# Optimization experiments

Measured on AMD Instinct MI355X. Metric: run time of the kernel, lower is better.

Reference implementation:

```python
import jax, jax.numpy as jnp
import numpy as np

NUM_SITES = 64
BOND_DIM = 64
PHYS_DIM = 2
BATCH = 8192
INIT_STD = 0.125  # 1/sqrt(bond_dim)
EPS_AMP = 1e-12
EPS_LOG = 1e-30


def setup_inputs() -> dict:
    key = jax.random.key(0)
    k_cfg, k_l, k_b, k_r = jax.random.split(key, 4)
    configurations = jax.random.randint(k_cfg, (BATCH, NUM_SITES), 0, PHYS_DIM, dtype=jnp.int32)
    left = jax.random.normal(k_l, (PHYS_DIM, BOND_DIM), dtype=jnp.float32) * INIT_STD
    bulk = jax.random.normal(k_b, (NUM_SITES - 2, BOND_DIM, PHYS_DIM, BOND_DIM), dtype=jnp.float32) * INIT_STD
    right = jax.random.normal(k_r, (BOND_DIM, PHYS_DIM), dtype=jnp.float32) * INIT_STD
    return {"configurations": configurations, "left": left, "bulk": bulk, "right": right}


def _psi(configurations, left, bulk, right):
    # configurations: [B, S] int; left: [d, D]; bulk: [S-2, D, d, D]; right: [D, d]
    B = configurations.shape[0]
    env0 = left[configurations[:, 0]]  # [B, D]
    cfg_mid = configurations[:, 1:-1].T  # [S-2, B]

    def step(env, xs):
        site_t, idx = xs  # site_t: [D, d, D], idx: [B]
        D = site_t.shape[0]
        # env @ site (contract left bond), then gather the per-sample physical slice
        tmp = (env @ site_t.reshape(D, -1)).reshape(B, PHYS_DIM, D)  # [B, d, D]
        env = jnp.take_along_axis(tmp, idx[:, None, None], axis=1)[:, 0, :]  # [B, D]
        return env, None

    env, _ = jax.lax.scan(step, env0, (bulk, cfg_mid))
    cols = jnp.take(right, configurations[:, -1], axis=1).T  # [B, D]
    return jnp.sum(env * cols, axis=1)  # [B]


def _log_norm(left, bulk, right):
    env0 = left.T @ left  # [D, D]  (real dtype -> conj trivial)

    def step(carry, site_t):
        env, log_scale = carry
        sm = jnp.transpose(site_t, (1, 0, 2))  # [d, D, D]
        env = jnp.einsum('pdi,de,pej->ij', sm, env, sm)  # sum_p A_p^H env A_p
        scale = jnp.maximum(jnp.max(jnp.abs(env)), EPS_LOG)
        return (env / scale, log_scale + jnp.log(scale)), None

    (env, log_scale), _ = jax.lax.scan(step, (env0, jnp.zeros((), left.dtype)), bulk)
    z = jnp.sum(right * (env @ right))
    return jnp.log(jnp.maximum(z, EPS_LOG)) + log_scale


def reference(configurations, left, bulk, right):
    psi = _psi(configurations, left, bulk, right)
    abs_sq = jnp.maximum(psi * psi, EPS_AMP)
    log_z = _log_norm(left, bulk, right)
    nll = -(jnp.log(abs_sq) - log_z)
    return jnp.mean(nll)
```

## Files before the change

kernel.cpp:

```cpp
#include <hip/hip_runtime.h>
#include <math.h>

#define NBULK 62
#define SB    72
#define NPSI  128
#define NBLK  130

typedef __attribute__((ext_vector_type(8))) short bf8_t;
typedef __attribute__((ext_vector_type(4))) float f4_t;

#define MFMA(a, b, c) __builtin_amdgcn_mfma_f32_16x16x32_bf16((a), (b), (c), 0, 0, 0)

__device__ __forceinline__ unsigned short f2bf(float f) {
    unsigned int u = __float_as_uint(f);
    return (unsigned short)((u + 0x7FFFu + ((u >> 16) & 1u)) >> 16);
}
__device__ __forceinline__ float bf2f(unsigned short h) {
    return __uint_as_float(((unsigned int)h) << 16);
}

#define WS_E_OFF   1024
#define WS_B_OFF   6144
#define WS_BT_OFF  45056
#define WS_MR_OFF  1060864


extern "C" __global__ __launch_bounds__(256)
void mps_precompute(const float* __restrict__ bulkG,
                    unsigned short* __restrict__ BTg,
                    unsigned short* __restrict__ MRg,
                    float* __restrict__ wsF)
{
    __shared__ unsigned short BTl[8192];
    __shared__ unsigned short MRl[8192];
    const int s = blockIdx.x, tid = threadIdx.x;
    if (s == 0 && tid == 0) {
        wsF[0] = 0.f; wsF[1] = 0.f; wsF[2] = 0.f;
        ((int*)wsF)[3] = 0;
    }
    const float4* src = (const float4*)(bulkG + (size_t)s * 8192);
    for (int c = 0; c < 8; ++c) {
        int idx = tid + c * 256;
        float4 v = src[idx];
        int f  = idx * 4;
        int kk = f >> 7;
        int p  = (f >> 6) & 1;
        int j  = f & 63;
        unsigned short b0 = f2bf(v.x), b1 = f2bf(v.y), b2 = f2bf(v.z), b3 = f2bf(v.w);
        int n = p * 64 + kk;
        int off = n * 64 + (((j >> 3) ^ (n & 7)) << 3) + (j & 7);
        MRl[off + 0] = b0; MRl[off + 1] = b1; MRl[off + 2] = b2; MRl[off + 3] = b3;
        unsigned short bb[4] = {b0, b1, b2, b3};
        #pragma unroll
        for (int t2 = 0; t2 < 4; ++t2) {
            int n2 = p * 64 + j + t2;
            BTl[n2 * 64 + (((kk >> 3) ^ (n2 & 7)) << 3) + (kk & 7)] = bb[t2];
        }
    }
    __syncthreads();
    const uint4* bt4 = (const uint4*)BTl;
    const uint4* mr4 = (const uint4*)MRl;
    uint4* btg = (uint4*)(BTg + (size_t)s * 8192);
    uint4* mrg = (uint4*)(MRg + (size_t)s * 8192);
    for (int c = 0; c < 4; ++c) {
        int idx = tid + c * 256;
        btg[idx] = bt4[idx];
        mrg[idx] = mr4[idx];
    }
}

extern "C" __global__ __launch_bounds__(256, 1)
void mps_main(const int* __restrict__ cfgG, const float* __restrict__ leftG,
              const float* __restrict__ rightG, float* __restrict__ wsF,
              const unsigned short* __restrict__ BTg,
              const unsigned short* __restrict__ MRg,
              float* __restrict__ outG)
{
    extern __shared__ char smem[];
    unsigned short* smem16 = (unsigned short*)smem;
    const int tid  = threadIdx.x;
    const int bid  = blockIdx.x;
    const int wv   = tid >> 6;
    const int lane = tid & 63;
    const int quad = lane >> 4;
    const int ln   = lane & 15;

    if (bid >= 2) {
        unsigned short* env  = smem16;
        unsigned char*  selT = (unsigned char*)(env + 64 * SB);

        const int s0 = (bid - 2) * 64;
        {
            int m = tid >> 2, part = tid & 3;
            const int* row = cfgG + (size_t)(s0 + m) * 64 + part * 16;
            #pragma unroll
            for (int q = 0; q < 4; ++q) {
                int4 v = *(const int4*)(row + q * 4);
                int cb = part * 16 + q * 4;
                selT[(cb + 0) * 64 + m] = (unsigned char)v.x;
                selT[(cb + 1) * 64 + m] = (unsigned char)v.y;
                selT[(cb + 2) * 64 + m] = (unsigned char)v.z;
                selT[(cb + 3) * 64 + m] = (unsigned char)v.w;
            }
        }
        __syncthreads();

        int boff[2][4][2];
        #pragma unroll
        for (int b2 = 0; b2 < 2; ++b2)
            #pragma unroll
            for (int ct = 0; ct < 4; ++ct) {
                int row = b2 * 64 + ct * 16 + ln;
                #pragma unroll
                for (int h = 0; h < 2; ++h)
                    boff[b2][ct][h] = row * 64 + (((h * 4 + quad) ^ (ln & 7)) << 3);
            }

        bf8_t Af0, Af1;
        {
            int sel0 = selT[0 * 64 + wv * 16 + ln];
            const float* lp0 = leftG + sel0 * 64;
            bf8_t t0, t1;
            #pragma unroll
            for (int j = 0; j < 8; ++j) {
                t0[j] = (short)f2bf(lp0[quad * 8 + j]);
                t1[j] = (short)f2bf(lp0[32 + quad * 8 + j]);
            }
            Af0 = t0; Af1 = t1;
        }

        auto loadB = [&](bf8_t (&B)[2][4][2], int t) {
            const unsigned short* base = BTg + (size_t)t * 8192;
            #pragma unroll
            for (int b2 = 0; b2 < 2; ++b2)
                #pragma unroll
                for (int ct = 0; ct < 4; ++ct)
                    #pragma unroll
                    for (int h = 0; h < 2; ++h)
                        B[b2][ct][h] = *(const bf8_t*)(base + boff[b2][ct][h]);
        };
        auto psite = [&](bf8_t (&B)[2][4][2], int t) {
            f4_t acc[2][4];
            #pragma unroll
            for (int b2 = 0; b2 < 2; ++b2)
                #pragma unroll
                for (int ct = 0; ct < 4; ++ct) {
                    f4_t a = {0.f, 0.f, 0.f, 0.f};
                    a = MFMA(Af0, B[b2][ct][0], a);
                    a = MFMA(Af1, B[b2][ct][1], a);
                    acc[b2][ct] = a;
                }
            unsigned int sv = *(const unsigned int*)(selT + (t + 1) * 64 + wv * 16 + quad * 4);
            #pragma unroll
            for (int ct = 0; ct < 4; ++ct)
                #pragma unroll
                for (int r = 0; r < 4; ++r) {
                    float v = ((sv >> (8 * r)) & 1u) ? acc[1][ct][r] : acc[0][ct][r];
                    env[(wv * 16 + quad * 4 + r) * SB + ct * 16 + ln] = f2bf(v);
                }
            Af0 = *(const bf8_t*)(env + (wv * 16 + ln) * SB + quad * 8);
            Af1 = *(const bf8_t*)(env + (wv * 16 + ln) * SB + 32 + quad * 8);
        };

        bf8_t BfA[2][4][2], BfB[2][4][2];
        loadB(BfA, 0);
        for (int tt = 0; tt < 31; ++tt) {
            loadB(BfB, 2 * tt + 1);
            psite(BfA, 2 * tt);
            if (tt < 30) loadB(BfA, 2 * tt + 2);
            psite(BfB, 2 * tt + 1);
        }
        {
            int selL = selT[63 * 64 + wv * 16 + ln];
            bf8_t e0 = *(const bf8_t*)(env + (wv * 16 + ln) * SB + quad * 16);
            bf8_t e1 = *(const bf8_t*)(env + (wv * 16 + ln) * SB + quad * 16 + 8);
            float p = 0.f;
            #pragma unroll
            for (int j = 0; j < 8; ++j)
                p = fmaf(bf2f((unsigned short)e0[j]), rightG[(quad * 16 + j) * 2 + selL], p);
            #pragma unroll
            for (int j = 0; j < 8; ++j)
                p = fmaf(bf2f((unsigned short)e1[j]), rightG[(quad * 16 + 8 + j) * 2 + selL], p);
            p += __shfl_xor(p, 16);
            p += __shfl_xor(p, 32);
            float lp = logf(fmaxf(p * p, 1e-12f));
            lp += __shfl_xor(lp, 1); lp += __shfl_xor(lp, 2);
            lp += __shfl_xor(lp, 4); lp += __shfl_xor(lp, 8);
            if (lane == 0) atomicAdd(&wsF[0], lp);
        }
    } else {
        unsigned short* Ebf = smem16;
        unsigned short* St0 = Ebf + 64 * SB;
        unsigned short* St1 = St0 + 64 * SB;
        float* wred = (float*)(St1 + 64 * SB);

        const bool fwd = (bid == 0);
        const unsigned short* srcbase = fwd ? BTg : MRg;
        {
            int i = tid >> 2, jq = tid & 3;
            for (int jj = 0; jj < 16; ++jj) {
                int j = jq * 16 + jj;
                float v;
                if (fwd) v = leftG[i] * leftG[j] + leftG[64 + i] * leftG[64 + j];
                else     v = rightG[i * 2] * rightG[j * 2] + rightG[i * 2 + 1] * rightG[j * 2 + 1];
                Ebf[i * SB + j] = f2bf(v);
            }
        }
        float lsum = 0.f;
        const int p   = wv >> 1;
        const int ntb = (wv & 1) * 2;
        const int mta = (wv >> 1) * 2;
        const int nta = (wv & 1) * 2;
        unsigned short* Stp = p ? St1 : St0;

        int o1[2][2], o2[2][2][2];
        #pragma unroll
        for (int c = 0; c < 2; ++c) {
            int row = p * 64 + (ntb + c) * 16 + ln;
            #pragma unroll
            for (int h = 0; h < 2; ++h)
                o1[c][h] = row * 64 + (((h * 4 + quad) ^ (ln & 7)) << 3);
        }
        #pragma unroll
        for (int pp = 0; pp < 2; ++pp)
            #pragma unroll
            for (int mi = 0; mi < 2; ++mi) {
                int row = pp * 64 + (mta + mi) * 16 + ln;
                #pragma unroll
                for (int h = 0; h < 2; ++h)
                    o2[pp][mi][h] = row * 64 + (((h * 4 + quad) ^ (ln & 7)) << 3);
            }

        auto loadM = [&](bf8_t (&M1)[2][2], bf8_t (&M2)[2][2][2], int site) {
            const unsigned short* base = srcbase + (size_t)site * 8192;
            #pragma unroll
            for (int c = 0; c < 2; ++c)
                #pragma unroll
                for (int h = 0; h < 2; ++h)
                    M1[c][h] = *(const bf8_t*)(base + o1[c][h]);
            #pragma unroll
            for (int pp = 0; pp < 2; ++pp)
                #pragma unroll
                for (int mi = 0; mi < 2; ++mi)
                    #pragma unroll
                    for (int h = 0; h < 2; ++h)
                        M2[pp][mi][h] = *(const bf8_t*)(base + o2[pp][mi][h]);
        };
        auto nsite = [&](bf8_t (&M1)[2][2], bf8_t (&M2)[2][2][2],
                         bf8_t (&N1)[2][2], bf8_t (&N2)[2][2][2], int k, bool pf) {
            __syncthreads();
            float inv = 1.f;
            if (k > 0) {
                const float* wp = wred + ((k - 1) & 1) * 4;
                float mm = fmaxf(fmaxf(wp[0], wp[1]), fmaxf(wp[2], wp[3]));
                float sc = fmaxf(mm, 1e-30f);
                inv = 1.f / sc;
                if (tid == 0) lsum += logf(sc);
            }
            if (pf) loadM(N1, N2, fwd ? (k + 1) : (61 - (k + 1)));
            {
                bf8_t Af2[4][2];
                #pragma unroll
                for (int mt = 0; mt < 4; ++mt)
                    #pragma unroll
                    for (int h = 0; h < 2; ++h)
                        Af2[mt][h] = *(const bf8_t*)(Ebf + (mt * 16 + ln) * SB + h * 32 + quad * 8);
                #pragma unroll
                for (int c = 0; c < 2; ++c) {
                    int nt = ntb + c;
                    #pragma unroll
                    for (int mt = 0; mt < 4; ++mt) {
                        f4_t a = {0.f, 0.f, 0.f, 0.f};
                        a = MFMA(Af2[mt][0], M1[c][0], a);
                        a = MFMA(Af2[mt][1], M1[c][1], a);
                        ushort4 pk;
                        pk.x = f2bf(a[0]); pk.y = f2bf(a[1]); pk.z = f2bf(a[2]); pk.w = f2bf(a[3]);
                        *(ushort4*)(Stp + (nt * 16 + ln) * SB + mt * 16 + quad * 4) = pk;
                    }
                }
            }
            __syncthreads();
            {
                bf8_t Bw[2][2][2];
                #pragma unroll
                for (int pp = 0; pp < 2; ++pp)
                    #pragma unroll
                    for (int ni = 0; ni < 2; ++ni)
                        #pragma unroll
                        for (int h = 0; h < 2; ++h)
                            Bw[pp][ni][h] = *(const bf8_t*)((pp ? St1 : St0)
                                            + ((nta + ni) * 16 + ln) * SB + h * 32 + quad * 8);
                float mx = 0.f;
                #pragma unroll
                for (int mi = 0; mi < 2; ++mi)
                    #pragma unroll
                    for (int ni = 0; ni < 2; ++ni) {
                        f4_t a = {0.f, 0.f, 0.f, 0.f};
                        #pragma unroll
                        for (int pp = 0; pp < 2; ++pp)
                            #pragma unroll
                            for (int h = 0; h < 2; ++h)
                                a = MFMA(M2[pp][mi][h], Bw[pp][ni][h], a);
                        #pragma unroll
                        for (int r = 0; r < 4; ++r) {
                            float val = a[r] * inv;
                            mx = fmaxf(mx, fabsf(val));
                            Ebf[((mta + mi) * 16 + quad * 4 + r) * SB + (nta + ni) * 16 + ln] = f2bf(val);
                        }
                    }
                #pragma unroll
                for (int off = 32; off > 0; off >>= 1)
                    mx = fmaxf(mx, __shfl_xor(mx, off));
                if (lane == 0) wred[(k & 1) * 4 + wv] = mx;
            }
        };

        bf8_t M1A[2][2], M2A[2][2][2], M1B[2][2], M2B[2][2][2];
        loadM(M1A, M2A, fwd ? 0 : 61);
        for (int kk = 0; kk < 15; ++kk) {
            nsite(M1A, M2A, M1B, M2B, 2 * kk,     true);
            nsite(M1B, M2B, M1A, M2A, 2 * kk + 1, true);
        }
        nsite(M1A, M2A, M1B, M2B, 30, false);

        __syncthreads();
        float* dst = wsF + (fwd ? WS_E_OFF : WS_B_OFF);
        for (int c = 0; c < 16; ++c) {
            int idx = tid + c * 256;
            dst[idx] = bf2f(Ebf[(idx >> 6) * SB + (idx & 63)]);
        }
        if (tid == 0) wsF[fwd ? 1 : 2] = lsum;
    }

    __syncthreads();
    __threadfence();
    __syncthreads();
    int* eflag = (int*)smem;
    if (tid == 0) {
        int old = atomicAdd((int*)wsF + 3, 1);
        eflag[0] = (old == NBLK - 1) ? 1 : 0;
    }
    __syncthreads();
    if (eflag[0]) {
        __threadfence();
        const float4* E  = (const float4*)(wsF + WS_E_OFF);
        const float4* Bm = (const float4*)(wsF + WS_B_OFF);
        float a = 0.f;
        #pragma unroll
        for (int c = 0; c < 4; ++c) {
            int idx = tid + c * 256;
            float4 e = E[idx], b = Bm[idx];
            a += e.x * b.x + e.y * b.y + e.z * b.z + e.w * b.w;
        }
        #pragma unroll
        for (int off = 32; off > 0; off >>= 1)
            a += __shfl_down(a, off);
        float* ered = (float*)smem + 8;
        if ((tid & 63) == 0) ered[tid >> 6] = a;
        __syncthreads();
        if (tid == 0) {
            float z = fmaxf(ered[0] + ered[1] + ered[2] + ered[3], 1e-30f);
            float log_z = logf(z) + wsF[1] + wsF[2];
            outG[0] = log_z - wsF[0] * (1.0f / 8192.0f);
        }
    }
}

extern "C" void kernel_launch(void* const* d_in, const int* in_sizes, int n_in,
                              void* d_out, int out_size, void* d_ws, size_t ws_size,
                              hipStream_t stream)
{
    const int*   cfg   = (const int*)d_in[0];
    const float* left  = (const float*)d_in[1];
    const float* bulk  = (const float*)d_in[2];
    const float* right = (const float*)d_in[3];
    float* wsF = (float*)d_ws;
    unsigned short* BTg = (unsigned short*)((char*)d_ws + WS_BT_OFF);
    unsigned short* MRg = (unsigned short*)((char*)d_ws + WS_MR_OFF);

    mps_precompute<<<dim3(62), dim3(256), 0, stream>>>(bulk, BTg, MRg, wsF);
    mps_main<<<dim3(NBLK), dim3(256), 28672, stream>>>(cfg, left, right, wsF, BTg, MRg, (float*)d_out);
}
```

Before: 123.0 us.

## Pre-multiply adjacent MPS site pairs to halve sequential contraction steps

A precompute kernel now multiplies pairs of adjacent bulk tensors into four 64x64 product matrices per pair (one per physical index combination), so the psi chain and the norm chain each take 31 or fewer sequential steps instead of 62. The psi blocks stage each pair tile through LDS with register prefetch and select among four products using a combined 2-bit selector. The norm blocks contract over four physical combinations per step. This removes half of the latency-bound serial steps at the cost of twice the MFMA work per step, an extra bf16 rounding of the pair products (a precision change), and a larger LDS footprint.

```diff
diff --git a/kernel.cpp b/kernel.cpp
--- a/kernel.cpp
+++ b/kernel.cpp
@@ -1,15 +1,14 @@
 #include <hip/hip_runtime.h>
 #include <math.h>
 
-#define NBULK 62
-#define SB    72
-#define NPSI  128
+#define NPAIR 31
 #define NBLK  130
 
 typedef __attribute__((ext_vector_type(8))) short bf8_t;
 typedef __attribute__((ext_vector_type(4))) float f4_t;
 
 #define MFMA(a, b, c) __builtin_amdgcn_mfma_f32_16x16x32_bf16((a), (b), (c), 0, 0, 0)
+#define LGKM_BARRIER() asm volatile("s_waitcnt lgkmcnt(0)\n\ts_barrier" ::: "memory")
 
 __device__ __forceinline__ unsigned short f2bf(float f) {
     unsigned int u = __float_as_uint(f);
@@ -19,61 +18,90 @@
     return __uint_as_float(((unsigned int)h) << 16);
 }
 
-#define WS_E_OFF   1024
-#define WS_B_OFF   6144
-#define WS_BT_OFF  45056
-#define WS_MR_OFF  1060864
-
+#define WS_E_OFF 1024
+#define WS_B_OFF 6144
+#define WS_PBT   45056
+#define WS_PMR   1060864
 
 extern "C" __global__ __launch_bounds__(256)
-void mps_precompute(const float* __restrict__ bulkG,
-                    unsigned short* __restrict__ BTg,
-                    unsigned short* __restrict__ MRg,
-                    float* __restrict__ wsF)
+void mps_pre(const float* __restrict__ bulkG, unsigned short* __restrict__ PBTg,
+             unsigned short* __restrict__ PMRg, float* __restrict__ wsF)
 {
-    __shared__ unsigned short BTl[8192];
-    __shared__ unsigned short MRl[8192];
-    const int s = blockIdx.x, tid = threadIdx.x;
-    if (s == 0 && tid == 0) {
-        wsF[0] = 0.f; wsF[1] = 0.f; wsF[2] = 0.f;
-        ((int*)wsF)[3] = 0;
+    extern __shared__ char smem[];
+    unsigned short* S = (unsigned short*)smem;
+    const int t = blockIdx.x, tid = threadIdx.x;
+    const int wv = tid >> 6, lane = tid & 63, quad = lane >> 4, ln = lane & 15;
+    if (t == 0 && tid == 0) { wsF[0] = 0.f; wsF[1] = 0.f; wsF[2] = 0.f; ((int*)wsF)[3] = 0; }
+
+    unsigned short* Arow = S;
+    unsigned short* Bbt  = S + 8192;
+    const float4* sA = (const float4*)(bulkG + (size_t)(2 * t) * 8192);
+    const float4* sB = (const float4*)(bulkG + (size_t)(2 * t + 1) * 8192);
+    for (int it = 0; it < 8; ++it) {
+        int idx = tid + it * 256;
+        int f = idx * 4, kk = f >> 7, p = (f >> 6) & 1, j = f & 63;
+        float4 va = sA[idx];
+        ushort4 pa; pa.x = f2bf(va.x); pa.y = f2bf(va.y); pa.z = f2bf(va.z); pa.w = f2bf(va.w);
+        *(ushort4*)(Arow + p * 4096 + kk * 64 + (((j >> 3) ^ (kk & 7)) << 3) + (j & 7)) = pa;
+        float4 vb = sB[idx];
+        unsigned short bb[4] = {f2bf(vb.x), f2bf(vb.y), f2bf(vb.z), f2bf(vb.w)};
+        #pragma unroll
+        for (int r2 = 0; r2 < 4; ++r2) {
+            int n = j + r2;
+            Bbt[p * 4096 + n * 64 + (((kk >> 3) ^ (n & 7)) << 3) + (kk & 7)] = bb[r2];
+        }
     }
-    const float4* src = (const float4*)(bulkG + (size_t)s * 8192);
-    for (int c = 0; c < 8; ++c) {
-        int idx = tid + c * 256;
-        float4 v = src[idx];
-        int f  = idx * 4;
-        int kk = f >> 7;
-        int p  = (f >> 6) & 1;
-        int j  = f & 63;
-        unsigned short b0 = f2bf(v.x), b1 = f2bf(v.y), b2 = f2bf(v.z), b3 = f2bf(v.w);
-        int n = p * 64 + kk;
-        int off = n * 64 + (((j >> 3) ^ (n & 7)) << 3) + (j & 7);
-        MRl[off + 0] = b0; MRl[off + 1] = b1; MRl[off + 2] = b2; MRl[off + 3] = b3;
-        unsigned short bb[4] = {b0, b1, b2, b3};
-        #pragma unroll
-        for (int t2 = 0; t2 < 4; ++t2) {
-            int n2 = p * 64 + j + t2;
-            BTl[n2 * 64 + (((kk >> 3) ^ (n2 & 7)) << 3) + (kk & 7)] = bb[t2];
-        }
-    }
-    __syncthreads();
-    const uint4* bt4 = (const uint4*)BTl;
-    const uint4* mr4 = (const uint4*)MRl;
-    uint4* btg = (uint4*)(BTg + (size_t)s * 8192);
-    uint4* mrg = (uint4*)(MRg + (size_t)s * 8192);
-    for (int c = 0; c < 4; ++c) {
-        int idx = tid + c * 256;
-        btg[idx] = bt4[idx];
-        mrg[idx] = mr4[idx];
+    __syncthreads();
+    const int a = wv & 1, b = wv >> 1;
+    bf8_t Af[4][2], Bf[4][2];
+    #pragma unroll
+    for (int mt = 0; mt < 4; ++mt)
+        #pragma unroll
+        for (int h = 0; h < 2; ++h) {
+            Af[mt][h] = *(const bf8_t*)(Arow + a * 4096 + (mt * 16 + ln) * 64 + (((h * 4 + quad) ^ (ln & 7)) << 3));
+            Bf[mt][h] = *(const bf8_t*)(Bbt  + b * 4096 + (mt * 16 + ln) * 64 + (((h * 4 + quad) ^ (ln & 7)) << 3));
+        }
+    __syncthreads();
+    f4_t acc[4][4];
+    #pragma unroll
+    for (int mt = 0; mt < 4; ++mt)
+        #pragma unroll
+        for (int nt = 0; nt < 4; ++nt) {
+            f4_t x = {0.f, 0.f, 0.f, 0.f};
+            x = MFMA(Af[mt][0], Bf[nt][0], x);
+            x = MFMA(Af[mt][1], Bf[nt][1], x);
+            acc[mt][nt] = x;
+        }
+    unsigned short* Pr = S;
+    unsigned short* Pt = S + 16384;
+    #pragma unroll
+    for (int mt = 0; mt < 4; ++mt)
+        #pragma unroll
+        for (int nt = 0; nt < 4; ++nt)
+            #pragma unroll
+            for (int r = 0; r < 4; ++r) {
+                int row = mt * 16 + quad * 4 + r, col = nt * 16 + ln;
+                unsigned short v = f2bf(acc[mt][nt][r]);
+                Pr[wv * 4096 + row * 64 + (((col >> 3) ^ (row & 7)) << 3) + (col & 7)] = v;
+                Pt[wv * 4096 + col * 64 + (((row >> 3) ^ (col & 7)) << 3) + (row & 7)] = v;
+            }
+    __syncthreads();
+    const uint4* pr4 = (const uint4*)Pr;
+    const uint4* pt4 = (const uint4*)Pt;
+    uint4* mr = (uint4*)(PMRg + (size_t)t * 16384);
+    uint4* bt = (uint4*)(PBTg + (size_t)t * 16384);
+    for (int it = 0; it < 8; ++it) {
+        int idx = tid + it * 256;
+        mr[idx] = pr4[idx];
+        bt[idx] = pt4[idx];
     }
 }
 
 extern "C" __global__ __launch_bounds__(256, 1)
 void mps_main(const int* __restrict__ cfgG, const float* __restrict__ leftG,
               const float* __restrict__ rightG, float* __restrict__ wsF,
-              const unsigned short* __restrict__ BTg,
-              const unsigned short* __restrict__ MRg,
+              const unsigned short* __restrict__ PBTg,
+              const unsigned short* __restrict__ PMRg,
               float* __restrict__ outG)
 {
     extern __shared__ char smem[];
@@ -86,8 +114,10 @@
     const int ln   = lane & 15;
 
     if (bid >= 2) {
-        unsigned short* env  = smem16;
-        unsigned char*  selT = (unsigned char*)(env + 64 * SB);
+        unsigned short* tile = smem16;
+        unsigned short* env  = tile + 16384;
+        unsigned char*  selT = (unsigned char*)(env + 4096);
+        unsigned char*  selP = selT + 4096;
 
         const int s0 = (bid - 2) * 64;
         {
@@ -104,21 +134,13 @@
             }
         }
         __syncthreads();
-
-        int boff[2][4][2];
-        #pragma unroll
-        for (int b2 = 0; b2 < 2; ++b2)
-            #pragma unroll
-            for (int ct = 0; ct < 4; ++ct) {
-                int row = b2 * 64 + ct * 16 + ln;
-                #pragma unroll
-                for (int h = 0; h < 2; ++h)
-                    boff[b2][ct][h] = row * 64 + (((h * 4 + quad) ^ (ln & 7)) << 3);
-            }
-
+        for (int idx = tid; idx < NPAIR * 64; idx += 256) {
+            int pt2 = idx >> 6, m = idx & 63;
+            selP[idx] = (unsigned char)(selT[(2 * pt2 + 1) * 64 + m] + 2 * selT[(2 * pt2 + 2) * 64 + m]);
+        }
         bf8_t Af0, Af1;
         {
-            int sel0 = selT[0 * 64 + wv * 16 + ln];
+            int sel0 = selT[wv * 16 + ln];
             const float* lp0 = leftG + sel0 * 64;
             bf8_t t0, t1;
             #pragma unroll
@@ -128,52 +150,62 @@
             }
             Af0 = t0; Af1 = t1;
         }
-
-        auto loadB = [&](bf8_t (&B)[2][4][2], int t) {
-            const unsigned short* base = BTg + (size_t)t * 8192;
-            #pragma unroll
-            for (int b2 = 0; b2 < 2; ++b2)
-                #pragma unroll
-                for (int ct = 0; ct < 4; ++ct)
-                    #pragma unroll
-                    for (int h = 0; h < 2; ++h)
-                        B[b2][ct][h] = *(const bf8_t*)(base + boff[b2][ct][h]);
-        };
-        auto psite = [&](bf8_t (&B)[2][4][2], int t) {
-            f4_t acc[2][4];
-            #pragma unroll
-            for (int b2 = 0; b2 < 2; ++b2)
+        uint4 pf[8];
+        {
+            const uint4* g0 = (const uint4*)PBTg;
+            #pragma unroll
+            for (int c = 0; c < 8; ++c)
+                pf[c] = g0[(wv * 8 + c) * 64 + lane];
+        }
+
+        for (int t = 0; t < NPAIR; ++t) {
+            LGKM_BARRIER();
+            {
+                uint4* tl4 = (uint4*)tile;
+                #pragma unroll
+                for (int c = 0; c < 8; ++c)
+                    tl4[(wv * 8 + c) * 64 + lane] = pf[c];
+            }
+            LGKM_BARRIER();
+            if (t + 1 < NPAIR) {
+                const uint4* gn = (const uint4*)(PBTg + (size_t)(t + 1) * 16384);
+                #pragma unroll
+                for (int c = 0; c < 8; ++c)
+                    pf[c] = gn[(wv * 8 + c) * 64 + lane];
+            }
+            f4_t acc[4][4];
+            #pragma unroll
+            for (int c = 0; c < 4; ++c)
                 #pragma unroll
                 for (int ct = 0; ct < 4; ++ct) {
-                    f4_t a = {0.f, 0.f, 0.f, 0.f};
-                    a = MFMA(Af0, B[b2][ct][0], a);
-                    a = MFMA(Af1, B[b2][ct][1], a);
-                    acc[b2][ct] = a;
+                    const unsigned short* rb = tile + c * 4096 + (ct * 16 + ln) * 64;
+                    bf8_t b0 = *(const bf8_t*)(rb + ((quad ^ (ln & 7)) << 3));
+                    bf8_t b1 = *(const bf8_t*)(rb + (((4 + quad) ^ (ln & 7)) << 3));
+                    f4_t x = {0.f, 0.f, 0.f, 0.f};
+                    x = MFMA(Af0, b0, x);
+                    x = MFMA(Af1, b1, x);
+                    acc[c][ct] = x;
                 }
-            unsigned int sv = *(const unsigned int*)(selT + (t + 1) * 64 + wv * 16 + quad * 4);
+            unsigned int sv = *(const unsigned int*)(selP + t * 64 + wv * 16 + quad * 4);
             #pragma unroll
             for (int ct = 0; ct < 4; ++ct)
                 #pragma unroll
                 for (int r = 0; r < 4; ++r) {
-                    float v = ((sv >> (8 * r)) & 1u) ? acc[1][ct][r] : acc[0][ct][r];
-                    env[(wv * 16 + quad * 4 + r) * SB + ct * 16 + ln] = f2bf(v);
+                    unsigned int bs = (sv >> (8 * r)) & 3u;
+                    float v01 = (bs & 1u) ? acc[1][ct][r] : acc[0][ct][r];
+                    float v23 = (bs & 1u) ? acc[3][ct][r] : acc[2][ct][r];
+                    float v   = (bs & 2u) ? v23 : v01;
+                    int row = wv * 16 + quad * 4 + r;
+                    env[row * 64 + (((ct * 2 + (ln >> 3)) ^ (row & 7)) << 3) + (ln & 7)] = f2bf(v);
                 }
-            Af0 = *(const bf8_t*)(env + (wv * 16 + ln) * SB + quad * 8);
-            Af1 = *(const bf8_t*)(env + (wv * 16 + ln) * SB + 32 + quad * 8);
-        };
-
-        bf8_t BfA[2][4][2], BfB[2][4][2];
-        loadB(BfA, 0);
-        for (int tt = 0; tt < 31; ++tt) {
-            loadB(BfB, 2 * tt + 1);
-            psite(BfA, 2 * tt);
-            if (tt < 30) loadB(BfA, 2 * tt + 2);
-            psite(BfB, 2 * tt + 1);
-        }
-        {
-            int selL = selT[63 * 64 + wv * 16 + ln];
-            bf8_t e0 = *(const bf8_t*)(env + (wv * 16 + ln) * SB + quad * 16);
-            bf8_t e1 = *(const bf8_t*)(env + (wv * 16 + ln) * SB + quad * 16 + 8);
+            Af0 = *(const bf8_t*)(env + (wv * 16 + ln) * 64 + ((quad ^ (ln & 7)) << 3));
+            Af1 = *(const bf8_t*)(env + (wv * 16 + ln) * 64 + (((4 + quad) ^ (ln & 7)) << 3));
+        }
+        {
+            int row = wv * 16 + ln;
+            int selL = selT[63 * 64 + row];
+            bf8_t e0 = *(const bf8_t*)(env + row * 64 + (((quad * 2) ^ (row & 7)) << 3));
+            bf8_t e1 = *(const bf8_t*)(env + row * 64 + (((quad * 2 + 1) ^ (row & 7)) << 3));
             float p = 0.f;
             #pragma unroll
             for (int j = 0; j < 8; ++j)
@@ -190,12 +222,12 @@
         }
     } else {
         unsigned short* Ebf = smem16;
-        unsigned short* St0 = Ebf + 64 * SB;
-        unsigned short* St1 = St0 + 64 * SB;
-        float* wred = (float*)(St1 + 64 * SB);
+        unsigned short* Sst = Ebf + 4096;
+        float* wred = (float*)(Sst + 16384);
 
         const bool fwd = (bid == 0);
-        const unsigned short* srcbase = fwd ? BTg : MRg;
+        const int NP = fwd ? 16 : 15;
+        const unsigned short* srcbase = fwd ? PBTg : PMRg;
         {
             int i = tid >> 2, jq = tid & 3;
             for (int jj = 0; jj < 16; ++jj) {
@@ -203,52 +235,39 @@
                 float v;
                 if (fwd) v = leftG[i] * leftG[j] + leftG[64 + i] * leftG[64 + j];
                 else     v = rightG[i * 2] * rightG[j * 2] + rightG[i * 2 + 1] * rightG[j * 2 + 1];
-                Ebf[i * SB + j] = f2bf(v);
+                Ebf[i * 64 + (((j >> 3) ^ (i & 7)) << 3) + (j & 7)] = f2bf(v);
             }
         }
         float lsum = 0.f;
-        const int p   = wv >> 1;
-        const int ntb = (wv & 1) * 2;
         const int mta = (wv >> 1) * 2;
         const int nta = (wv & 1) * 2;
-        unsigned short* Stp = p ? St1 : St0;
-
-        int o1[2][2], o2[2][2][2];
-        #pragma unroll
-        for (int c = 0; c < 2; ++c) {
-            int row = p * 64 + (ntb + c) * 16 + ln;
+
+        int o1[4][2], o2[4][2][2];
+        #pragma unroll
+        for (int nt = 0; nt < 4; ++nt)
             #pragma unroll
             for (int h = 0; h < 2; ++h)
-                o1[c][h] = row * 64 + (((h * 4 + quad) ^ (ln & 7)) << 3);
-        }
-        #pragma unroll
-        for (int pp = 0; pp < 2; ++pp)
-            #pragma unroll
-            for (int mi = 0; mi < 2; ++mi) {
-                int row = pp * 64 + (mta + mi) * 16 + ln;
+                o1[nt][h] = wv * 4096 + (nt * 16 + ln) * 64 + (((h * 4 + quad) ^ (ln & 7)) << 3);
+        #pragma unroll
+        for (int c = 0; c < 4; ++c)
+            #pragma unroll
+            for (int mi = 0; mi < 2; ++mi)
                 #pragma unroll
                 for (int h = 0; h < 2; ++h)
-                    o2[pp][mi][h] = row * 64 + (((h * 4 + quad) ^ (ln & 7)) << 3);
-            }
-
-        auto loadM = [&](bf8_t (&M1)[2][2], bf8_t (&M2)[2][2][2], int site) {
-            const unsigned short* base = srcbase + (size_t)site * 8192;
-            #pragma unroll
-            for (int c = 0; c < 2; ++c)
+                    o2[c][mi][h] = c * 4096 + ((mta + mi) * 16 + ln) * 64 + (((h * 4 + quad) ^ (ln & 7)) << 3);
+
+        bf8_t Bc0[4][2], Bc1[4][2];
+        {
+            const unsigned short* base = srcbase + (size_t)(fwd ? 0 : 30) * 16384;
+            #pragma unroll
+            for (int nt = 0; nt < 4; ++nt)
                 #pragma unroll
                 for (int h = 0; h < 2; ++h)
-                    M1[c][h] = *(const bf8_t*)(base + o1[c][h]);
-            #pragma unroll
-            for (int pp = 0; pp < 2; ++pp)
-                #pragma unroll
-                for (int mi = 0; mi < 2; ++mi)
-                    #pragma unroll
-                    for (int h = 0; h < 2; ++h)
-                        M2[pp][mi][h] = *(const bf8_t*)(base + o2[pp][mi][h]);
-        };
-        auto nsite = [&](bf8_t (&M1)[2][2], bf8_t (&M2)[2][2][2],
-                         bf8_t (&N1)[2][2], bf8_t (&N2)[2][2][2], int k, bool pf) {
-            __syncthreads();
+                    Bc0[nt][h] = *(const bf8_t*)(base + o1[nt][h]);
+        }
+
+        for (int k = 0; k < NP; ++k) {
+            LGKM_BARRIER();
             float inv = 1.f;
             if (k > 0) {
                 const float* wp = wred + ((k - 1) & 1) * 4;
@@ -257,55 +276,76 @@
                 inv = 1.f / sc;
                 if (tid == 0) lsum += logf(sc);
             }
-            if (pf) loadM(N1, N2, fwd ? (k + 1) : (61 - (k + 1)));
+            bf8_t Aw[4][2][2];
             {
-                bf8_t Af2[4][2];
-                #pragma unroll
-                for (int mt = 0; mt < 4; ++mt)
+                const unsigned short* base = srcbase + (size_t)(fwd ? k : (30 - k)) * 16384;
+                #pragma unroll
+                for (int c = 0; c < 4; ++c)
+                    #pragma unroll
+                    for (int mi = 0; mi < 2; ++mi)
+                        #pragma unroll
+                        for (int h = 0; h < 2; ++h)
+                            Aw[c][mi][h] = *(const bf8_t*)(base + o2[c][mi][h]);
+            }
+            bf8_t (&Bcur)[4][2] = (k & 1) ? Bc1 : Bc0;
+            if (k + 1 < NP) {
+                bf8_t (&Bnxt)[4][2] = (k & 1) ? Bc0 : Bc1;
+                const unsigned short* base = srcbase + (size_t)(fwd ? (k + 1) : (30 - (k + 1))) * 16384;
+                #pragma unroll
+                for (int nt = 0; nt < 4; ++nt)
                     #pragma unroll
                     for (int h = 0; h < 2; ++h)
-                        Af2[mt][h] = *(const bf8_t*)(Ebf + (mt * 16 + ln) * SB + h * 32 + quad * 8);
-                #pragma unroll
-                for (int c = 0; c < 2; ++c) {
-                    int nt = ntb + c;
+                        Bnxt[nt][h] = *(const bf8_t*)(base + o1[nt][h]);
+            }
+            {
+                unsigned short* SstW = Sst + wv * 4096;
+                #pragma unroll
+                for (int mt = 0; mt < 4; ++mt) {
+                    const unsigned short* er = Ebf + (mt * 16 + ln) * 64;
+                    bf8_t a0 = *(const bf8_t*)(er + ((quad ^ (ln & 7)) << 3));
+                    bf8_t a1 = *(const bf8_t*)(er + (((4 + quad) ^ (ln & 7)) << 3));
                     #pragma unroll
-                    for (int mt = 0; mt < 4; ++mt) {
-                        f4_t a = {0.f, 0.f, 0.f, 0.f};
-                        a = MFMA(Af2[mt][0], M1[c][0], a);
-                        a = MFMA(Af2[mt][1], M1[c][1], a);
+                    for (int nt = 0; nt < 4; ++nt) {
+                        f4_t x = {0.f, 0.f, 0.f, 0.f};
+                        x = MFMA(a0, Bcur[nt][0], x);
+                        x = MFMA(a1, Bcur[nt][1], x);
+                        int n = nt * 16 + ln;
+                        int dg = mt * 2 + (quad >> 1);
                         ushort4 pk;
-                        pk.x = f2bf(a[0]); pk.y = f2bf(a[1]); pk.z = f2bf(a[2]); pk.w = f2bf(a[3]);
-                        *(ushort4*)(Stp + (nt * 16 + ln) * SB + mt * 16 + quad * 4) = pk;
+                        pk.x = f2bf(x[0]); pk.y = f2bf(x[1]); pk.z = f2bf(x[2]); pk.w = f2bf(x[3]);
+                        *(ushort4*)(SstW + n * 64 + ((dg ^ (n & 7)) << 3) + (quad & 1) * 4) = pk;
                     }
                 }
             }
-            __syncthreads();
+            LGKM_BARRIER();
             {
-                bf8_t Bw[2][2][2];
-                #pragma unroll
-                for (int pp = 0; pp < 2; ++pp)
+                bf8_t Bw[4][2][2];
+                #pragma unroll
+                for (int c = 0; c < 4; ++c)
                     #pragma unroll
                     for (int ni = 0; ni < 2; ++ni)
                         #pragma unroll
                         for (int h = 0; h < 2; ++h)
-                            Bw[pp][ni][h] = *(const bf8_t*)((pp ? St1 : St0)
-                                            + ((nta + ni) * 16 + ln) * SB + h * 32 + quad * 8);
+                            Bw[c][ni][h] = *(const bf8_t*)(Sst + c * 4096 + ((nta + ni) * 16 + ln) * 64
+                                                           + (((h * 4 + quad) ^ (ln & 7)) << 3));
                 float mx = 0.f;
                 #pragma unroll
                 for (int mi = 0; mi < 2; ++mi)
                     #pragma unroll
                     for (int ni = 0; ni < 2; ++ni) {
-                        f4_t a = {0.f, 0.f, 0.f, 0.f};
+                        f4_t x = {0.f, 0.f, 0.f, 0.f};
                         #pragma unroll
-                        for (int pp = 0; pp < 2; ++pp)
-                            #pragma unroll
-                            for (int h = 0; h < 2; ++h)
-                                a = MFMA(M2[pp][mi][h], Bw[pp][ni][h], a);
+                        for (int c = 0; c < 4; ++c) {
+                            x = MFMA(Aw[c][mi][0], Bw[c][ni][0], x);
+                            x = MFMA(Aw[c][mi][1], Bw[c][ni][1], x);
+                        }
                         #pragma unroll
                         for (int r = 0; r < 4; ++r) {
-                            float val = a[r] * inv;
+                            float val = x[r] * inv;
                             mx = fmaxf(mx, fabsf(val));
-                            Ebf[((mta + mi) * 16 + quad * 4 + r) * SB + (nta + ni) * 16 + ln] = f2bf(val);
+                            int row = (mta + mi) * 16 + quad * 4 + r;
+                            int col = (nta + ni) * 16 + ln;
+                            Ebf[row * 64 + (((col >> 3) ^ (row & 7)) << 3) + (col & 7)] = f2bf(val);
                         }
                     }
                 #pragma unroll
@@ -313,21 +353,13 @@
                     mx = fmaxf(mx, __shfl_xor(mx, off));
                 if (lane == 0) wred[(k & 1) * 4 + wv] = mx;
             }
-        };
-
-        bf8_t M1A[2][2], M2A[2][2][2], M1B[2][2], M2B[2][2][2];
-        loadM(M1A, M2A, fwd ? 0 : 61);
-        for (int kk = 0; kk < 15; ++kk) {
-            nsite(M1A, M2A, M1B, M2B, 2 * kk,     true);
-            nsite(M1B, M2B, M1A, M2A, 2 * kk + 1, true);
-        }
-        nsite(M1A, M2A, M1B, M2B, 30, false);
-
+        }
         __syncthreads();
         float* dst = wsF + (fwd ? WS_E_OFF : WS_B_OFF);
         for (int c = 0; c < 16; ++c) {
             int idx = tid + c * 256;
-            dst[idx] = bf2f(Ebf[(idx >> 6) * SB + (idx & 63)]);
+            int i = idx >> 6, j = idx & 63;
+            dst[idx] = bf2f(Ebf[i * 64 + (((j >> 3) ^ (i & 7)) << 3) + (j & 7)]);
         }
         if (tid == 0) wsF[fwd ? 1 : 2] = lsum;
     }
@@ -375,9 +407,9 @@
     const float* bulk  = (const float*)d_in[2];
     const float* right = (const float*)d_in[3];
     float* wsF = (float*)d_ws;
-    unsigned short* BTg = (unsigned short*)((char*)d_ws + WS_BT_OFF);
-    unsigned short* MRg = (unsigned short*)((char*)d_ws + WS_MR_OFF);
-
-    mps_precompute<<<dim3(62), dim3(256), 0, stream>>>(bulk, BTg, MRg, wsF);
-    mps_main<<<dim3(NBLK), dim3(256), 28672, stream>>>(cfg, left, right, wsF, BTg, MRg, (float*)d_out);
+    unsigned short* PBTg = (unsigned short*)((char*)d_ws + WS_PBT);
+    unsigned short* PMRg = (unsigned short*)((char*)d_ws + WS_PMR);
+
+    mps_pre<<<dim3(NPAIR), dim3(256), 65536, stream>>>(bulk, PBTg, PMRg, wsF);
+    mps_main<<<dim3(NBLK), dim3(256), 47104, stream>>>(cfg, left, right, wsF, PBTg, PMRg, (float*)d_out);
 }
```

Result: slower. 167.2 us (+35.9%).
